# Performance work log

Measured on AMD Instinct MI355X. Metric: run time of the kernel, lower is better.

## Reference

```python
import jax, jax.numpy as jnp
import numpy as np

N_TOKENS = 4096
HIDDEN = 1024
FFN = 2048
N_EXPERTS = 8
TOP_K = 2


def setup_inputs() -> dict:
    key = jax.random.key(0)
    k1, k2, k3, k4 = jax.random.split(key, 4)
    x = jax.random.normal(k1, (N_TOKENS, HIDDEN), dtype=jnp.float32)
    router_weight = jax.random.normal(k2, (HIDDEN, N_EXPERTS), dtype=jnp.float32)
    # matches torch.randn(...) * 0.02 init scale
    w1 = jax.random.normal(k3, (HIDDEN, FFN * N_EXPERTS), dtype=jnp.float32) * 0.02
    w2 = jax.random.normal(k4, (FFN * N_EXPERTS, HIDDEN), dtype=jnp.float32) * 0.02
    return {"x": x, "router_weight": router_weight, "w1": w1, "w2": w2, "top_k": TOP_K}


def reference(x, router_weight, w1, w2, top_k):
    # x: [N, H]; router_weight: [H, E]; w1: [H, E*F]; w2: [E*F, H]
    N, H = x.shape
    E = router_weight.shape[1]
    F = w1.shape[1] // E

    # --- routing (router in fp32, softmax over experts, top-k probs) ---
    logits = x.astype(jnp.float32) @ router_weight            # [N, E]
    probs = jax.nn.softmax(logits, axis=-1)                   # [N, E]
    topk_probs, topk_idx = jax.lax.top_k(probs, top_k)        # [N, k]

    # --- expert FFN: per-expert gelu(x @ w1_e) @ w2_e ---
    # Dense formulation: compute every expert for every token, then gather the
    # top-k outputs per token. Same math as grouped-GEMM dispatch/combine.
    h = jax.nn.gelu(x @ w1, approximate=False)                # [N, E*F]
    h = h.reshape(N, E, F)
    w2e = w2.reshape(E, F, H)
    y = jnp.einsum('nef,efh->neh', h, w2e)                    # [N, E, H]

    # --- combine: weight selected expert outputs by router probs, sum top-k ---
    sel = jnp.take_along_axis(y, topk_idx[:, :, None], axis=1)   # [N, k, H]
    out = (sel * topk_probs[:, :, None].astype(sel.dtype)).sum(axis=1)  # [N, H]
    return out
```

## Files before the change

### kernel.cpp

```cpp
#include <hip/hip_runtime.h>
#include <hip/hip_bf16.h>
#include <math.h>

#define N_TOK 4096
#define HID   1024
#define FFN   2048
#define NEXP  8
#define WROW  (NEXP*FFN)
#define NSLOT (N_TOK*2)
#define NCHUNK (NSLOT/64)

typedef __attribute__((ext_vector_type(4))) float f32x4;
typedef __attribute__((ext_vector_type(8))) short short8;

__device__ inline unsigned short f2bf(float f) {
  union { float f; unsigned u; } v; v.f = f;
  unsigned r = v.u + 0x7fffu + ((v.u >> 16) & 1u);
  return (unsigned short)(r >> 16);
}
__device__ __forceinline__ float bf2f(unsigned short u) {
  union { unsigned u; float f; } v; v.u = ((unsigned)u) << 16; return v.f;
}

__device__ __forceinline__ float gelu_f(float v) {
  const float u = 1.5957691216057308f * v + 0.07135481627f * (v * v * v);
  return v / (1.f + __expf(-u));
}

__device__ __forceinline__ void gload16(const void* g, void* l) {
  __builtin_amdgcn_global_load_lds((const __attribute__((address_space(1))) void*)g,
                                   (__attribute__((address_space(3))) void*)l, 16, 0, 0);
}


__global__ __launch_bounds__(256) void router_kernel(
    const float* __restrict__ x, const float* __restrict__ rw,
    int* __restrict__ eidx, float* __restrict__ probs,
    unsigned short* __restrict__ xb) {
  __shared__ float rwT[NEXP][HID];
  const int t = threadIdx.x;
  #pragma unroll
  for (int it = 0; it < 8; ++it) {
    const int flat = t * 4 + it * 1024;
    const f32x4 v = *(const f32x4*)&rw[flat];
    #pragma unroll
    for (int j = 0; j < 4; ++j) rwT[(flat + j) & 7][(flat + j) >> 3] = v[j];
  }
  __syncthreads();

  const int w = t >> 6, l = t & 63;
  const int n = blockIdx.x * 4 + w;
  const float* xr = x + (size_t)n * HID;
  float acc[NEXP];
  #pragma unroll
  for (int e = 0; e < NEXP; ++e) acc[e] = 0.f;

  #pragma unroll
  for (int j = 0; j < 4; ++j) {
    const int i = l * 4 + j * 256;
    const f32x4 xv = *(const f32x4*)&xr[i];
    if (xb) {
      ushort4 o;
      o.x = f2bf(xv[0]); o.y = f2bf(xv[1]); o.z = f2bf(xv[2]); o.w = f2bf(xv[3]);
      *(ushort4*)&xb[(size_t)n * HID + i] = o;
    }
    #pragma unroll
    for (int e = 0; e < NEXP; ++e) {
      const f32x4 wv = *(const f32x4*)&rwT[e][i];
      acc[e] += xv[0] * wv[0] + xv[1] * wv[1] + xv[2] * wv[2] + xv[3] * wv[3];
    }
  }
  #pragma unroll
  for (int e = 0; e < NEXP; ++e) {
    float s = acc[e];
    #pragma unroll
    for (int off = 32; off; off >>= 1) s += __shfl_xor(s, off);
    acc[e] = s;
  }
  if (l == 0) {
    float m = acc[0];
    #pragma unroll
    for (int e = 1; e < NEXP; ++e) m = fmaxf(m, acc[e]);
    float p[NEXP]; float den = 0.f;
    #pragma unroll
    for (int e = 0; e < NEXP; ++e) { p[e] = expf(acc[e] - m); den += p[e]; }
    const float inv = 1.f / den;
    int e1 = 0; float b1 = -1.f;
    #pragma unroll
    for (int e = 0; e < NEXP; ++e) if (p[e] > b1) { b1 = p[e]; e1 = e; }
    int e2 = 0; float b2 = -1.f;
    #pragma unroll
    for (int e = 0; e < NEXP; ++e) if (e != e1 && p[e] > b2) { b2 = p[e]; e2 = e; }
    eidx[n * 2 + 0] = e1; eidx[n * 2 + 1] = e2;
    probs[n * 2 + 0] = b1 * inv; probs[n * 2 + 1] = b2 * inv;
  }
}

__global__ __launch_bounds__(256) void dispatch_kernel(
    const int* __restrict__ eidx, const float* __restrict__ probs,
    int* __restrict__ counts, int* __restrict__ offs,
    int* __restrict__ rowtok, float* __restrict__ rowprob,
    int* __restrict__ tokslot) {
  __shared__ int chunkbase[NCHUNK][NEXP];
  __shared__ int tot[NEXP], off_s[NEXP];
  const int t = threadIdx.x;
  const int w = t >> 6, l = t & 63;

  for (int c = w; c < NCHUNK; c += 4) {
    const int e = eidx[c * 64 + l];
    #pragma unroll
    for (int xp = 0; xp < NEXP; ++xp) {
      const unsigned long long m = __ballot(e == xp);
      if (l == xp) chunkbase[c][xp] = __popcll(m);
    }
  }
  __syncthreads();

  if (t < NEXP) {
    int a = 0;
    for (int c = 0; c < NCHUNK; ++c) {
      const int v = chunkbase[c][t];
      chunkbase[c][t] = a;
      a += v;
    }
    tot[t] = a;
  }
  __syncthreads();
  if (t == 0) {
    int a = 0;
    for (int e = 0; e < NEXP; ++e) { off_s[e] = a; offs[e] = a; counts[e] = tot[e]; a += tot[e]; }
  }
  __syncthreads();

  for (int c = w; c < NCHUNK; c += 4) {
    const int s = c * 64 + l;
    const int e = eidx[s];
    unsigned long long mask_e = 0;
    #pragma unroll
    for (int xp = 0; xp < NEXP; ++xp) {
      const unsigned long long m = __ballot(e == xp);
      if (e == xp) mask_e = m;
    }
    const unsigned long long below = mask_e & ((1ull << l) - 1ull);
    const int pos = off_s[e] + chunkbase[c][e] + __popcll(below);
    rowtok[pos]  = s >> 1;
    rowprob[pos] = probs[s];
    tokslot[s]   = pos;
  }
}

__global__ __launch_bounds__(256) void tconv_kernel(
    const float* __restrict__ in, unsigned short* __restrict__ out,
    int R, int C, int RB) {
  __shared__ float tile[64][65];
  const int r0 = blockIdx.y * 64, c0 = blockIdx.x * 64;
  const int t = threadIdx.x;
  const int tr = t >> 4;
  const int tc4 = (t & 15) * 4;
  #pragma unroll
  for (int i = 0; i < 4; ++i) {
    const int r = tr + i * 16;
    const f32x4 v = *(const f32x4*)&in[(size_t)(r0 + r) * C + c0 + tc4];
    tile[r][tc4 + 0] = v[0]; tile[r][tc4 + 1] = v[1];
    tile[r][tc4 + 2] = v[2]; tile[r][tc4 + 3] = v[3];
  }
  __syncthreads();
  const int eb  = r0 / RB;
  const int rm0 = r0 % RB;
  #pragma unroll
  for (int i = 0; i < 4; ++i) {
    const int c = tr + i * 16;
    ushort4 o;
    o.x = f2bf(tile[tc4 + 0][c]); o.y = f2bf(tile[tc4 + 1][c]);
    o.z = f2bf(tile[tc4 + 2][c]); o.w = f2bf(tile[tc4 + 3][c]);
    const size_t oidx = (size_t)eb * C * RB + (size_t)(c0 + c) * RB + rm0 + tc4;
    *(ushort4*)&out[oidx] = o;
  }
}

__global__ __launch_bounds__(256) void gemm1_fast(
    const unsigned short* __restrict__ xb, const unsigned short* __restrict__ w1t,
    const int* __restrict__ rowtok, const int* __restrict__ counts,
    const int* __restrict__ offs, unsigned short* __restrict__ h1) {
  const int e   = blockIdx.z;
  const int cnt = counts[e];
  const int m0  = blockIdx.y * 128;
  if (m0 >= cnt) return;
  const int n0  = blockIdx.x * 128;
  const int seg = offs[e];

  __shared__ alignas(16) unsigned short Al[2][128 * 32];
  __shared__ alignas(16) unsigned short Bl[2][128 * 32];

  const int t  = threadIdx.x;
  const int l  = t & 63;
  const int w  = t >> 6;
  const int wr = w >> 1, wc = w & 1;
  const int lr = l & 15, hi = l >> 4;

  const int rowS = t >> 2;
  const int kc   = (((t & 3) ^ ((t >> 3) & 3)) * 8);
  const int ra0 = m0 + rowS      < cnt ? m0 + rowS      : cnt - 1;
  const int ra1 = m0 + rowS + 64 < cnt ? m0 + rowS + 64 : cnt - 1;
  const unsigned short* aptr0 = xb + (size_t)rowtok[seg + ra0] * HID + kc;
  const unsigned short* aptr1 = xb + (size_t)rowtok[seg + ra1] * HID + kc;
  const unsigned short* bptr0 = w1t + ((size_t)e * FFN + n0 + rowS)      * HID + kc;
  const unsigned short* bptr1 = w1t + ((size_t)e * FFN + n0 + rowS + 64) * HID + kc;
  const int ldst = (t & 192) * 8;
  const int koff = (hi ^ ((lr >> 1) & 3)) * 8;

  f32x4 acc[4][4];
  #pragma unroll
  for (int i = 0; i < 4; ++i)
    #pragma unroll
    for (int j = 0; j < 4; ++j) acc[i][j] = (f32x4){0.f, 0.f, 0.f, 0.f};

  auto STAGE = [&](int b, int k0) {
    gload16(aptr0 + k0, &Al[b][ldst]);
    gload16(aptr1 + k0, &Al[b][ldst + 2048]);
    gload16(bptr0 + k0, &Bl[b][ldst]);
    gload16(bptr1 + k0, &Bl[b][ldst + 2048]);
  };
  auto COMPUTE = [&](int b) {
    short8 af[4], bfr[4];
    #pragma unroll
    for (int mi = 0; mi < 4; ++mi) af[mi]  = *(const short8*)&Al[b][(wr * 64 + mi * 16 + lr) * 32 + koff];
    #pragma unroll
    for (int ni = 0; ni < 4; ++ni) bfr[ni] = *(const short8*)&Bl[b][(wc * 64 + ni * 16 + lr) * 32 + koff];
    #pragma unroll
    for (int mi = 0; mi < 4; ++mi)
      #pragma unroll
      for (int ni = 0; ni < 4; ++ni)
        acc[mi][ni] = __builtin_amdgcn_mfma_f32_16x16x32_bf16(af[mi], bfr[ni], acc[mi][ni], 0, 0, 0);
  };

  STAGE(0, 0);
  __syncthreads();
  for (int k0 = 0; k0 < HID; k0 += 64) {
    STAGE(1, k0 + 32);
    COMPUTE(0);
    __syncthreads();
    if (k0 + 64 < HID) STAGE(0, k0 + 64);
    COMPUTE(1);
    __syncthreads();
  }

  #pragma unroll
  for (int mi = 0; mi < 4; ++mi) {
    #pragma unroll
    for (int r = 0; r < 4; ++r) {
      const int grow = m0 + wr * 64 + mi * 16 + hi * 4 + r;
      if (grow < cnt) {
        const size_t rowoff = (size_t)(seg + grow) * FFN + n0 + wc * 64 + lr;
        #pragma unroll
        for (int ni = 0; ni < 4; ++ni)
          h1[rowoff + ni * 16] = f2bf(gelu_f(acc[mi][ni][r]));
      }
    }
  }
}

template<int KS>
__global__ __launch_bounds__(256) void gemm2_fast(
    const unsigned short* __restrict__ h1, const unsigned short* __restrict__ w2t,
    const int* __restrict__ counts, const int* __restrict__ offs,
    unsigned short* __restrict__ y) {
  const int e   = blockIdx.z & 7;
  const int kz  = blockIdx.z >> 3;
  const int cnt = counts[e];
  const int m0  = blockIdx.y * 128;
  if (m0 >= cnt) return;
  const int n0  = blockIdx.x * 128;
  const int seg = offs[e];
  constexpr int KLEN = FFN / KS;
  const int kbase = kz * KLEN;

  __shared__ alignas(16) unsigned short Al[2][128 * 32];
  __shared__ alignas(16) unsigned short Bl[2][128 * 32];

  const int t  = threadIdx.x;
  const int l  = t & 63;
  const int w  = t >> 6;
  const int wr = w >> 1, wc = w & 1;
  const int lr = l & 15, hi = l >> 4;

  const int rowS = t >> 2;
  const int kc   = (((t & 3) ^ ((t >> 3) & 3)) * 8);
  const int ra0 = m0 + rowS      < cnt ? m0 + rowS      : cnt - 1;
  const int ra1 = m0 + rowS + 64 < cnt ? m0 + rowS + 64 : cnt - 1;
  const unsigned short* aptr0 = h1 + (size_t)(seg + ra0) * FFN + kbase + kc;
  const unsigned short* aptr1 = h1 + (size_t)(seg + ra1) * FFN + kbase + kc;
  const unsigned short* bptr0 = w2t + ((size_t)e * HID + n0 + rowS)      * FFN + kbase + kc;
  const unsigned short* bptr1 = w2t + ((size_t)e * HID + n0 + rowS + 64) * FFN + kbase + kc;
  const int ldst = (t & 192) * 8;
  const int koff = (hi ^ ((lr >> 1) & 3)) * 8;

  f32x4 acc[4][4];
  #pragma unroll
  for (int i = 0; i < 4; ++i)
    #pragma unroll
    for (int j = 0; j < 4; ++j) acc[i][j] = (f32x4){0.f, 0.f, 0.f, 0.f};

  auto STAGE = [&](int b, int k0) {
    gload16(aptr0 + k0, &Al[b][ldst]);
    gload16(aptr1 + k0, &Al[b][ldst + 2048]);
    gload16(bptr0 + k0, &Bl[b][ldst]);
    gload16(bptr1 + k0, &Bl[b][ldst + 2048]);
  };
  auto COMPUTE = [&](int b) {
    short8 af[4], bfr[4];
    #pragma unroll
    for (int mi = 0; mi < 4; ++mi) af[mi]  = *(const short8*)&Al[b][(wr * 64 + mi * 16 + lr) * 32 + koff];
    #pragma unroll
    for (int ni = 0; ni < 4; ++ni) bfr[ni] = *(const short8*)&Bl[b][(wc * 64 + ni * 16 + lr) * 32 + koff];
    #pragma unroll
    for (int mi = 0; mi < 4; ++mi)
      #pragma unroll
      for (int ni = 0; ni < 4; ++ni)
        acc[mi][ni] = __builtin_amdgcn_mfma_f32_16x16x32_bf16(af[mi], bfr[ni], acc[mi][ni], 0, 0, 0);
  };

  STAGE(0, 0);
  __syncthreads();
  for (int k0 = 0; k0 < KLEN; k0 += 64) {
    STAGE(1, k0 + 32);
    COMPUTE(0);
    __syncthreads();
    if (k0 + 64 < KLEN) STAGE(0, k0 + 64);
    COMPUTE(1);
    __syncthreads();
  }

  #pragma unroll
  for (int mi = 0; mi < 4; ++mi) {
    #pragma unroll
    for (int r = 0; r < 4; ++r) {
      const int grow = m0 + wr * 64 + mi * 16 + hi * 4 + r;
      if (grow < cnt) {
        const int slot = seg + grow;
        unsigned short* yrow = y + ((size_t)kz * NSLOT + slot) * HID + n0 + wc * 64 + lr;
        #pragma unroll
        for (int ni = 0; ni < 4; ++ni)
          yrow[ni * 16] = f2bf(acc[mi][ni][r]);
      }
    }
  }
}

template<int KS>
__global__ __launch_bounds__(256) void combine_kernel(
    const unsigned short* __restrict__ y, const int* __restrict__ tokslot,
    const float* __restrict__ probs, float* __restrict__ out) {
  const int n = blockIdx.x;
  const int c = threadIdx.x * 4;
  const int s1 = tokslot[n * 2 + 0], s2 = tokslot[n * 2 + 1];
  const float p1 = probs[n * 2 + 0], p2 = probs[n * 2 + 1];
  float r0 = 0.f, r1 = 0.f, r2 = 0.f, r3 = 0.f;
  #pragma unroll
  for (int kz = 0; kz < KS; ++kz) {
    const ushort4 a = *(const ushort4*)&y[((size_t)kz * NSLOT + s1) * HID + c];
    const ushort4 b = *(const ushort4*)&y[((size_t)kz * NSLOT + s2) * HID + c];
    r0 += p1 * bf2f(a.x) + p2 * bf2f(b.x);
    r1 += p1 * bf2f(a.y) + p2 * bf2f(b.y);
    r2 += p1 * bf2f(a.z) + p2 * bf2f(b.z);
    r3 += p1 * bf2f(a.w) + p2 * bf2f(b.w);
  }
  *(f32x4*)&out[(size_t)n * HID + c] = (f32x4){r0, r1, r2, r3};
}

__global__ __launch_bounds__(256) void gemm2_fast_atomic(
    const unsigned short* __restrict__ h1, const unsigned short* __restrict__ w2t,
    const int* __restrict__ rowtok, const float* __restrict__ rowprob,
    const int* __restrict__ counts, const int* __restrict__ offs,
    float* __restrict__ out) {
  const int e   = blockIdx.z;
  const int cnt = counts[e];
  const int m0  = blockIdx.y * 128;
  if (m0 >= cnt) return;
  const int n0  = blockIdx.x * 128;
  const int seg = offs[e];

  __shared__ alignas(16) unsigned short Al[128 * 32];
  __shared__ alignas(16) unsigned short Bl[128 * 32];

  const int t  = threadIdx.x;
  const int l  = t & 63;
  const int w  = t >> 6;
  const int wr = w >> 1, wc = w & 1;
  const int lr = l & 15, hi = l >> 4;

  const int rowS = t >> 2;
  const int kc   = (((t & 3) ^ ((t >> 3) & 3)) * 8);
  const int ra0 = m0 + rowS      < cnt ? m0 + rowS      : cnt - 1;
  const int ra1 = m0 + rowS + 64 < cnt ? m0 + rowS + 64 : cnt - 1;
  const unsigned short* aptr0 = h1 + (size_t)(seg + ra0) * FFN + kc;
  const unsigned short* aptr1 = h1 + (size_t)(seg + ra1) * FFN + kc;
  const unsigned short* bptr0 = w2t + ((size_t)e * HID + n0 + rowS)      * FFN + kc;
  const unsigned short* bptr1 = w2t + ((size_t)e * HID + n0 + rowS + 64) * FFN + kc;
  unsigned short* const ldsA0 = Al + (t & 192) * 8;
  unsigned short* const ldsB0 = Bl + (t & 192) * 8;
  const int koff = (hi ^ ((lr >> 1) & 3)) * 8;

  f32x4 acc[4][4];
  #pragma unroll
  for (int i = 0; i < 4; ++i)
    #pragma unroll
    for (int j = 0; j < 4; ++j) acc[i][j] = (f32x4){0.f, 0.f, 0.f, 0.f};

  for (int k0 = 0; k0 < FFN; k0 += 32) {
    gload16(aptr0 + k0, ldsA0);
    gload16(aptr1 + k0, ldsA0 + 2048);
    gload16(bptr0 + k0, ldsB0);
    gload16(bptr1 + k0, ldsB0 + 2048);
    __syncthreads();
    short8 af[4], bfr[4];
    #pragma unroll
    for (int mi = 0; mi < 4; ++mi) af[mi]  = *(const short8*)&Al[(wr * 64 + mi * 16 + lr) * 32 + koff];
    #pragma unroll
    for (int ni = 0; ni < 4; ++ni) bfr[ni] = *(const short8*)&Bl[(wc * 64 + ni * 16 + lr) * 32 + koff];
    #pragma unroll
    for (int mi = 0; mi < 4; ++mi)
      #pragma unroll
      for (int ni = 0; ni < 4; ++ni)
        acc[mi][ni] = __builtin_amdgcn_mfma_f32_16x16x32_bf16(af[mi], bfr[ni], acc[mi][ni], 0, 0, 0);
    __syncthreads();
  }

  #pragma unroll
  for (int mi = 0; mi < 4; ++mi) {
    #pragma unroll
    for (int r = 0; r < 4; ++r) {
      const int grow = m0 + wr * 64 + mi * 16 + hi * 4 + r;
      if (grow < cnt) {
        const int slot = seg + grow;
        const int tok  = rowtok[slot];
        const float p  = rowprob[slot];
        #pragma unroll
        for (int ni = 0; ni < 4; ++ni)
          atomicAdd(&out[(size_t)tok * HID + n0 + wc * 64 + ni * 16 + lr], p * acc[mi][ni][r]);
      }
    }
  }
}

__global__ __launch_bounds__(256) void gemm1_old(
    const float* __restrict__ x, const float* __restrict__ w1,
    const int* __restrict__ rowtok, const int* __restrict__ counts,
    const int* __restrict__ offs, unsigned short* __restrict__ h1) {
  const int e   = blockIdx.z;
  const int cnt = counts[e];
  const int m0  = blockIdx.y * 64;
  if (m0 >= cnt) return;
  const int n0  = blockIdx.x * 64;
  const int seg = offs[e];
  __shared__ unsigned short Al[64 * 40];
  __shared__ unsigned short Bl[64 * 40];
  const int t  = threadIdx.x;
  const int l  = t & 63;
  const int wv = t >> 6;
  const int wr = wv >> 1, wc = wv & 1;
  const int am  = t >> 2;
  const int akb = (t & 3) * 8;
  const int amg = m0 + am;
  const bool aval = (amg < cnt);
  const float* aptr = aval ? (x + (size_t)rowtok[seg + amg] * HID + akb) : x;
  const int bn  = t & 63;
  const int bkg = (t >> 6) * 8;
  const float* bptr = w1 + (size_t)e * FFN + n0 + bn;
  f32x4 acc[2][2];
  #pragma unroll
  for (int i = 0; i < 2; ++i)
    #pragma unroll
    for (int j = 0; j < 2; ++j) acc[i][j] = (f32x4){0.f, 0.f, 0.f, 0.f};
  const int kreg = (l >> 4) * 8;
  const int lr   = l & 15;
  for (int k0 = 0; k0 < HID; k0 += 32) {
    short8 av = (short8){0,0,0,0,0,0,0,0};
    if (aval) {
      const f32x4 v0 = *(const f32x4*)(aptr + k0);
      const f32x4 v1 = *(const f32x4*)(aptr + k0 + 4);
      #pragma unroll
      for (int j = 0; j < 4; ++j) { av[j] = (short)f2bf(v0[j]); av[4 + j] = (short)f2bf(v1[j]); }
    }
    *(short8*)&Al[am * 40 + akb] = av;
    short8 bv;
    #pragma unroll
    for (int j = 0; j < 8; ++j) bv[j] = (short)f2bf(bptr[(size_t)(k0 + bkg + j) * WROW]);
    *(short8*)&Bl[bn * 40 + bkg] = bv;
    __syncthreads();
    short8 af[2], bfr[2];
    #pragma unroll
    for (int mi = 0; mi < 2; ++mi) af[mi]  = *(const short8*)&Al[(wr * 32 + mi * 16 + lr) * 40 + kreg];
    #pragma unroll
    for (int ni = 0; ni < 2; ++ni) bfr[ni] = *(const short8*)&Bl[(wc * 32 + ni * 16 + lr) * 40 + kreg];
    #pragma unroll
    for (int mi = 0; mi < 2; ++mi)
      #pragma unroll
      for (int ni = 0; ni < 2; ++ni)
        acc[mi][ni] = __builtin_amdgcn_mfma_f32_16x16x32_bf16(af[mi], bfr[ni], acc[mi][ni], 0, 0, 0);
    __syncthreads();
  }
  const int kq = l >> 4;
  #pragma unroll
  for (int mi = 0; mi < 2; ++mi) {
    #pragma unroll
    for (int r = 0; r < 4; ++r) {
      const int grow = m0 + wr * 32 + mi * 16 + kq * 4 + r;
      if (grow < cnt) {
        #pragma unroll
        for (int ni = 0; ni < 2; ++ni) {
          const float v = acc[mi][ni][r];
          const float g = 0.5f * v * (1.0f + erff(v * 0.70710678118654752f));
          h1[(size_t)(seg + grow) * FFN + n0 + wc * 32 + ni * 16 + lr] = f2bf(g);
        }
      }
    }
  }
}

__global__ __launch_bounds__(256) void gemm2_old(
    const unsigned short* __restrict__ h1, const float* __restrict__ w2,
    const int* __restrict__ rowtok, const float* __restrict__ rowprob,
    const int* __restrict__ counts, const int* __restrict__ offs,
    float* __restrict__ out) {
  const int e   = blockIdx.z;
  const int cnt = counts[e];
  const int m0  = blockIdx.y * 64;
  if (m0 >= cnt) return;
  const int n0  = blockIdx.x * 64;
  const int seg = offs[e];
  __shared__ unsigned short Al[64 * 40];
  __shared__ unsigned short Bl[64 * 40];
  const int t  = threadIdx.x;
  const int l  = t & 63;
  const int wv = t >> 6;
  const int wr = wv >> 1, wc = wv & 1;
  const int am  = t >> 2;
  const int akb = (t & 3) * 8;
  const int amg = m0 + am;
  const bool aval = (amg < cnt);
  const unsigned short* aptr = aval ? (h1 + (size_t)(seg + amg) * FFN + akb) : h1;
  const int bn  = t & 63;
  const int bkg = (t >> 6) * 8;
  const float* bptr = w2 + (size_t)e * FFN * HID + n0 + bn;
  f32x4 acc[2][2];
  #pragma unroll
  for (int i = 0; i < 2; ++i)
    #pragma unroll
    for (int j = 0; j < 2; ++j) acc[i][j] = (f32x4){0.f, 0.f, 0.f, 0.f};
  const int kreg = (l >> 4) * 8;
  const int lr   = l & 15;
  for (int k0 = 0; k0 < FFN; k0 += 32) {
    short8 av = (short8){0,0,0,0,0,0,0,0};
    if (aval) av = *(const short8*)(aptr + k0);
    *(short8*)&Al[am * 40 + akb] = av;
    short8 bv;
    #pragma unroll
    for (int j = 0; j < 8; ++j) bv[j] = (short)f2bf(bptr[(size_t)(k0 + bkg + j) * HID]);
    *(short8*)&Bl[bn * 40 + bkg] = bv;
    __syncthreads();
    short8 af[2], bfr[2];
    #pragma unroll
    for (int mi = 0; mi < 2; ++mi) af[mi]  = *(const short8*)&Al[(wr * 32 + mi * 16 + lr) * 40 + kreg];
    #pragma unroll
    for (int ni = 0; ni < 2; ++ni) bfr[ni] = *(const short8*)&Bl[(wc * 32 + ni * 16 + lr) * 40 + kreg];
    #pragma unroll
    for (int mi = 0; mi < 2; ++mi)
      #pragma unroll
      for (int ni = 0; ni < 2; ++ni)
        acc[mi][ni] = __builtin_amdgcn_mfma_f32_16x16x32_bf16(af[mi], bfr[ni], acc[mi][ni], 0, 0, 0);
    __syncthreads();
  }
  const int kq = l >> 4;
  #pragma unroll
  for (int mi = 0; mi < 2; ++mi) {
    #pragma unroll
    for (int r = 0; r < 4; ++r) {
      const int grow = m0 + wr * 32 + mi * 16 + kq * 4 + r;
      if (grow < cnt) {
        const int slot = seg + grow;
        const int tok  = rowtok[slot];
        const float p  = rowprob[slot];
        #pragma unroll
        for (int ni = 0; ni < 2; ++ni)
          atomicAdd(&out[(size_t)tok * HID + n0 + wc * 32 + ni * 16 + lr], p * acc[mi][ni][r]);
      }
    }
  }
}

extern "C" void kernel_launch(void* const* d_in, const int* in_sizes, int n_in,
                              void* d_out, int out_size, void* d_ws, size_t ws_size,
                              hipStream_t stream) {
  const float* x  = (const float*)d_in[0];
  const float* rw = (const float*)d_in[1];
  const float* w1 = (const float*)d_in[2];
  const float* w2 = (const float*)d_in[3];
  float* out = (float*)d_out;

  int*   counts  = (int*)d_ws;
  int*   offs    = counts + 8;
  int*   tokslot = counts + 16;
  int*   eidx    = tokslot + NSLOT;
  float* probs   = (float*)(eidx + NSLOT);
  int*   rowtok  = (int*)(probs + NSLOT);
  float* rowprob = (float*)(rowtok + NSLOT);
  unsigned short* h1 = (unsigned short*)(rowprob + NSLOT);
  unsigned short* xb = h1 + (size_t)NSLOT * FFN;
  unsigned short* wt = xb + (size_t)N_TOK * HID;
  unsigned short* y  = wt + (size_t)WROW * HID;

  const size_t need_base = (size_t)((char*)y - (char*)d_ws);
  const size_t need_y1   = need_base + (size_t)NSLOT * HID * 2;
  const size_t need_y2   = need_base + (size_t)2 * NSLOT * HID * 2;
  const bool fast = (ws_size >= need_base);

  router_kernel<<<N_TOK / 4, 256, 0, stream>>>(x, rw, eidx, probs, fast ? xb : nullptr);
  dispatch_kernel<<<1, 256, 0, stream>>>(eidx, probs, counts, offs, rowtok, rowprob, tokslot);

  if (fast) {
    tconv_kernel<<<dim3(WROW / 64, HID / 64), 256, 0, stream>>>(w1, wt, HID, WROW, HID);
    gemm1_fast<<<dim3(FFN / 128, NSLOT / 128, NEXP), 256, 0, stream>>>(xb, wt, rowtok, counts, offs, h1);
    tconv_kernel<<<dim3(HID / 64, WROW / 64), 256, 0, stream>>>(w2, wt, WROW, HID, FFN);
    if (ws_size >= need_y2) {
      gemm2_fast<2><<<dim3(HID / 128, NSLOT / 128, NEXP * 2), 256, 0, stream>>>(h1, wt, counts, offs, y);
      combine_kernel<2><<<N_TOK, 256, 0, stream>>>(y, tokslot, probs, out);
    } else if (ws_size >= need_y1) {
      gemm2_fast<1><<<dim3(HID / 128, NSLOT / 128, NEXP), 256, 0, stream>>>(h1, wt, counts, offs, y);
      combine_kernel<1><<<N_TOK, 256, 0, stream>>>(y, tokslot, probs, out);
    } else {
      hipMemsetAsync(d_out, 0, (size_t)out_size * sizeof(float), stream);
      gemm2_fast_atomic<<<dim3(HID / 128, NSLOT / 128, NEXP), 256, 0, stream>>>(h1, wt, rowtok, rowprob, counts, offs, out);
    }
  } else {
    hipMemsetAsync(d_out, 0, (size_t)out_size * sizeof(float), stream);
    gemm1_old<<<dim3(FFN / 64, NSLOT / 64, NEXP), 256, 0, stream>>>(x, w1, rowtok, counts, offs, h1);
    gemm2_old<<<dim3(HID / 64, NSLOT / 64, NEXP), 256, 0, stream>>>(h1, w2, rowtok, rowprob, counts, offs, out);
  }
}
```

Measured before the change: 218.5 us.

## Triple-buffer grouped GEMM LDS pipeline and remap workgroups across XCDs

Both grouped GEMMs switch from a two-stage LDS double buffer to a three-stage ring. Loads run two tiles ahead and are guarded by explicit vmcnt waits and a single barrier per 32-wide k-step, replacing two full __syncthreads per 64. Launch grids are flattened to 1D, and block ids are remapped so consecutive ids go to the same XCD chunk, improving L2 locality of shared weight and activation tiles. This uses 50% more LDS per block, which may lower occupancy. The hand-written waitcnt counts must match the number of loads issued per STAGE.

```diff
diff --git a/kernel.cpp b/kernel.cpp
--- a/kernel.cpp
+++ b/kernel.cpp
@@ -182,15 +182,20 @@
     const unsigned short* __restrict__ xb, const unsigned short* __restrict__ w1t,
     const int* __restrict__ rowtok, const int* __restrict__ counts,
     const int* __restrict__ offs, unsigned short* __restrict__ h1) {
-  const int e   = blockIdx.z;
+  int wg = blockIdx.x;
+  wg = (wg & 7) * (8192 / 8) + (wg >> 3);
+  const int bx = wg & 15;
+  const int by = (wg >> 4) & 63;
+  const int e  = wg >> 10;
+
   const int cnt = counts[e];
-  const int m0  = blockIdx.y * 128;
+  const int m0  = by * 128;
   if (m0 >= cnt) return;
-  const int n0  = blockIdx.x * 128;
+  const int n0  = bx * 128;
   const int seg = offs[e];
 
-  __shared__ alignas(16) unsigned short Al[2][128 * 32];
-  __shared__ alignas(16) unsigned short Bl[2][128 * 32];
+  __shared__ alignas(16) unsigned short Al[3][128 * 32];
+  __shared__ alignas(16) unsigned short Bl[3][128 * 32];
 
   const int t  = threadIdx.x;
   const int l  = t & 63;
@@ -234,15 +239,26 @@
         acc[mi][ni] = __builtin_amdgcn_mfma_f32_16x16x32_bf16(af[mi], bfr[ni], acc[mi][ni], 0, 0, 0);
   };
 
+  const int NT = HID / 32;
   STAGE(0, 0);
-  __syncthreads();
-  for (int k0 = 0; k0 < HID; k0 += 64) {
-    STAGE(1, k0 + 32);
-    COMPUTE(0);
-    __syncthreads();
-    if (k0 + 64 < HID) STAGE(0, k0 + 64);
-    COMPUTE(1);
-    __syncthreads();
+  STAGE(1, 32);
+  asm volatile("s_waitcnt vmcnt(4)" ::: "memory");
+  __builtin_amdgcn_s_barrier();
+  __builtin_amdgcn_sched_barrier(0);
+  int cur = 0;
+  for (int tt = 0; tt < NT; ++tt) {
+    if (tt + 2 < NT) {
+      int b2 = cur + 2; if (b2 >= 3) b2 -= 3;
+      STAGE(b2, (tt + 2) * 32);
+    }
+    COMPUTE(cur);
+    if (tt + 1 < NT) {
+      if (tt + 2 < NT) asm volatile("s_waitcnt vmcnt(4)" ::: "memory");
+      else             asm volatile("s_waitcnt vmcnt(0)" ::: "memory");
+      __builtin_amdgcn_s_barrier();
+      __builtin_amdgcn_sched_barrier(0);
+    }
+    ++cur; if (cur == 3) cur = 0;
   }
 
   #pragma unroll
@@ -265,18 +281,25 @@
     const unsigned short* __restrict__ h1, const unsigned short* __restrict__ w2t,
     const int* __restrict__ counts, const int* __restrict__ offs,
     unsigned short* __restrict__ y) {
-  const int e   = blockIdx.z & 7;
-  const int kz  = blockIdx.z >> 3;
+  constexpr int G = 8 * 64 * 8 * KS;
+  int wg = blockIdx.x;
+  wg = (wg & 7) * (G / 8) + (wg >> 3);
+  const int bx  = wg & 7;
+  const int by  = (wg >> 3) & 63;
+  const int bzz = wg >> 9;
+  const int e   = bzz & 7;
+  const int kz  = bzz >> 3;
+
   const int cnt = counts[e];
-  const int m0  = blockIdx.y * 128;
+  const int m0  = by * 128;
   if (m0 >= cnt) return;
-  const int n0  = blockIdx.x * 128;
+  const int n0  = bx * 128;
   const int seg = offs[e];
   constexpr int KLEN = FFN / KS;
   const int kbase = kz * KLEN;
 
-  __shared__ alignas(16) unsigned short Al[2][128 * 32];
-  __shared__ alignas(16) unsigned short Bl[2][128 * 32];
+  __shared__ alignas(16) unsigned short Al[3][128 * 32];
+  __shared__ alignas(16) unsigned short Bl[3][128 * 32];
 
   const int t  = threadIdx.x;
   const int l  = t & 63;
@@ -320,15 +343,26 @@
         acc[mi][ni] = __builtin_amdgcn_mfma_f32_16x16x32_bf16(af[mi], bfr[ni], acc[mi][ni], 0, 0, 0);
   };
 
+  const int NT = KLEN / 32;
   STAGE(0, 0);
-  __syncthreads();
-  for (int k0 = 0; k0 < KLEN; k0 += 64) {
-    STAGE(1, k0 + 32);
-    COMPUTE(0);
-    __syncthreads();
-    if (k0 + 64 < KLEN) STAGE(0, k0 + 64);
-    COMPUTE(1);
-    __syncthreads();
+  STAGE(1, 32);
+  asm volatile("s_waitcnt vmcnt(4)" ::: "memory");
+  __builtin_amdgcn_s_barrier();
+  __builtin_amdgcn_sched_barrier(0);
+  int cur = 0;
+  for (int tt = 0; tt < NT; ++tt) {
+    if (tt + 2 < NT) {
+      int b2 = cur + 2; if (b2 >= 3) b2 -= 3;
+      STAGE(b2, (tt + 2) * 32);
+    }
+    COMPUTE(cur);
+    if (tt + 1 < NT) {
+      if (tt + 2 < NT) asm volatile("s_waitcnt vmcnt(4)" ::: "memory");
+      else             asm volatile("s_waitcnt vmcnt(0)" ::: "memory");
+      __builtin_amdgcn_s_barrier();
+      __builtin_amdgcn_sched_barrier(0);
+    }
+    ++cur; if (cur == 3) cur = 0;
   }
 
   #pragma unroll
@@ -620,13 +654,13 @@
 
   if (fast) {
     tconv_kernel<<<dim3(WROW / 64, HID / 64), 256, 0, stream>>>(w1, wt, HID, WROW, HID);
-    gemm1_fast<<<dim3(FFN / 128, NSLOT / 128, NEXP), 256, 0, stream>>>(xb, wt, rowtok, counts, offs, h1);
+    gemm1_fast<<<16 * 64 * 8, 256, 0, stream>>>(xb, wt, rowtok, counts, offs, h1);
     tconv_kernel<<<dim3(HID / 64, WROW / 64), 256, 0, stream>>>(w2, wt, WROW, HID, FFN);
     if (ws_size >= need_y2) {
-      gemm2_fast<2><<<dim3(HID / 128, NSLOT / 128, NEXP * 2), 256, 0, stream>>>(h1, wt, counts, offs, y);
+      gemm2_fast<2><<<8 * 64 * 8 * 2, 256, 0, stream>>>(h1, wt, counts, offs, y);
       combine_kernel<2><<<N_TOK, 256, 0, stream>>>(y, tokslot, probs, out);
     } else if (ws_size >= need_y1) {
-      gemm2_fast<1><<<dim3(HID / 128, NSLOT / 128, NEXP), 256, 0, stream>>>(h1, wt, counts, offs, y);
+      gemm2_fast<1><<<8 * 64 * 8, 256, 0, stream>>>(h1, wt, counts, offs, y);
       combine_kernel<1><<<N_TOK, 256, 0, stream>>>(y, tokslot, probs, out);
     } else {
       hipMemsetAsync(d_out, 0, (size_t)out_size * sizeof(float), stream);
```

New measurement: 211.0 us. 1.04x faster.
